# Optimization experiments

Hardware: AMD Instinct MI355X
Metric: run time of the kernel (lower is better)

The kernel has to match this reference:

```python
import jax, jax.numpy as jnp
import numpy as np

KSIZE = 7
STRIDE = 4
SCALE = 10.0


def _same_pad(n, k, s):
    # torch 'same' padding used in extract_image_patches (asymmetric)
    out = -(-n // s)
    pad = max(0, (out - 1) * s + k - n)
    top = pad // 2
    return (top, pad - top)


def _conv1x1(x, W, b):
    # x: [C,H,W], W: [O,C], b: [O]
    return jnp.einsum('oc,chw->ohw', W, x) + b[:, None, None]


def _unfold(x, k, s, pad_h, pad_w):
    # x: [C,H,W] -> patches [Lh*Lw, C*k*k] in (C, kh, kw) order (torch Unfold order)
    C = x.shape[0]
    xp = jnp.pad(x, ((0, 0), pad_h, pad_w))
    Hp, Wp = xp.shape[1], xp.shape[2]
    Lh = (Hp - k) // s + 1
    Lw = (Wp - k) // s + 1
    ih = (jnp.arange(Lh) * s)[:, None] + jnp.arange(k)  # [Lh,k]
    iw = (jnp.arange(Lw) * s)[:, None] + jnp.arange(k)  # [Lw,k]
    p = xp[:, ih][:, :, :, iw]                # [C,Lh,k,Lw,k]
    p = p.transpose(1, 3, 0, 2, 4).reshape(Lh * Lw, C * k * k)
    return p, Lh, Lw


def _fold(p, Lh, Lw, C, k, s, H, W, pad):
    # p: [Lh*Lw, C*k*k] -> overlap-summed image [C,H,W] (torch F.fold, symmetric pad)
    P = p.reshape(Lh, Lw, C, k, k).transpose(2, 0, 1, 3, 4)  # [C,Lh,Lw,k,k]
    Hp, Wp = H + 2 * pad, W + 2 * pad
    ih = (jnp.arange(Lh) * s)[:, None] + jnp.arange(k)  # [Lh,k]
    iw = (jnp.arange(Lw) * s)[:, None] + jnp.arange(k)  # [Lw,k]
    IH = ih[:, None, :, None]  # broadcast -> [Lh,Lw,k,k]
    IW = iw[None, :, None, :]
    canvas = jnp.zeros((C, Hp, Wp), p.dtype).at[:, IH, IW].add(P)
    return canvas[:, pad:pad + H, pad:pad + W]


def _salsa_one(x, Wg, bg, Wt, bt, Wp, bp, Ww, bw):
    # x: [C,H,W]
    C, H, W = x.shape
    ic = Wg.shape[0]
    k, s = KSIZE, STRIDE
    ph = _same_pad(H, k, s)
    pw = _same_pad(W, k, s)
    q, Lh, Lw = _unfold(_conv1x1(x, Wg, bg), k, s, ph, pw)   # g   -> queries [L, ic*k*k]
    kk, _, _ = _unfold(_conv1x1(x, Wp, bp), k, s, ph, pw)    # phi -> keys
    v, _, _ = _unfold(_conv1x1(x, Wt, bt), k, s, ph, pw)     # theta -> values
    att = jax.nn.softmax((q @ kk.T) * SCALE, axis=1)         # [L1,L2]
    out = att @ v                                            # [L1, ic*k*k]
    fp = (k - 1) // 2  # paddings[0] from stride-1 same_padding in the original (=3)
    zi = _fold(out, Lh, Lw, ic, k, s, H, W, fp)
    ones_p, mLh, mLw = _unfold(jnp.ones((ic, H, W), x.dtype), k, s, (fp, fp), (fp, fp))
    mask = _fold(ones_p, mLh, mLw, ic, k, s, H, W, fp)
    zi = zi / mask
    return x + _conv1x1(zi, Ww, bw)


def setup_inputs() -> dict:
    key = jax.random.key(0)
    B, C, H, W, IC = 4, 64, 256, 256, 16
    ks = jax.random.split(key, 9)
    sC = 1.0 / np.sqrt(C)
    sI = 1.0 / np.sqrt(IC)
    return {
        'b': jax.random.normal(ks[0], (B, C, H, W), jnp.float32),
        'Wg': jax.random.normal(ks[1], (IC, C), jnp.float32) * sC,
        'bg': jax.random.normal(ks[2], (IC,), jnp.float32) * 0.01,
        'Wt': jax.random.normal(ks[3], (IC, C), jnp.float32) * sC,
        'bt': jax.random.normal(ks[4], (IC,), jnp.float32) * 0.01,
        'Wp': jax.random.normal(ks[5], (IC, C), jnp.float32) * sC,
        'bp': jax.random.normal(ks[6], (IC,), jnp.float32) * 0.01,
        'Ww': jax.random.normal(ks[7], (C, IC), jnp.float32) * sI,
        'bw': jax.random.normal(ks[8], (C,), jnp.float32) * 0.01,
    }


def reference(b, Wg, bg, Wt, bt, Wp, bp, Ww, bw):
    f = jax.vmap(_salsa_one, in_axes=(0, None, None, None, None, None, None, None, None))
    return f(b, Wg, bg, Wt, bt, Wp, bp, Ww, bw)
```

## Files before the change

kernel.cpp:

```cpp
#include <hip/hip_runtime.h>

#define CIN 64
#define ICN 16
#define HH 256
#define WID 256
#define HW (HH*WID)
#define LL 4096
#define KD 784
#define KDP 800
#define NVT 896
#define NB 4

typedef __attribute__((ext_vector_type(8))) short short8;
typedef __attribute__((ext_vector_type(4))) float f32x4;

__device__ __forceinline__ unsigned short f2bf(float x){
  union { float f; unsigned u; } v; v.f = x;
  unsigned r = v.u + 0x7FFF + ((v.u >> 16) & 1);
  return (unsigned short)(r >> 16);
}
__device__ __forceinline__ float bf2f(unsigned short h){
  union { unsigned u; float f; } v; v.u = ((unsigned)h) << 16; return v.f;
}

__global__ __launch_bounds__(256) void conv1x1_3(
    const float* __restrict__ x,
    const float* __restrict__ Wg, const float* __restrict__ bg,
    const float* __restrict__ Wp, const float* __restrict__ bp,
    const float* __restrict__ Wt, const float* __restrict__ bt,
    float* __restrict__ G, float* __restrict__ P, float* __restrict__ T) {
  __shared__ float wg[ICN*CIN], wp[ICN*CIN], wt[ICN*CIN];
  int t = threadIdx.x;
  for (int i = t; i < ICN*CIN; i += 256) { wg[i]=Wg[i]; wp[i]=Wp[i]; wt[i]=Wt[i]; }
  __syncthreads();
  int p = blockIdx.x*256 + t;
  float aG[ICN], aP[ICN], aT[ICN];
#pragma unroll
  for (int o=0;o<ICN;o++){ aG[o]=bg[o]; aP[o]=bp[o]; aT[o]=bt[o]; }
  for (int c=0;c<CIN;c++){
    float xv = x[c*HW + p];
#pragma unroll
    for (int o=0;o<ICN;o++){
      aG[o] = fmaf(wg[o*CIN+c], xv, aG[o]);
      aP[o] = fmaf(wp[o*CIN+c], xv, aP[o]);
      aT[o] = fmaf(wt[o*CIN+c], xv, aT[o]);
    }
  }
#pragma unroll
  for (int o=0;o<ICN;o++){ G[o*HW+p]=aG[o]; P[o*HW+p]=aP[o]; T[o*HW+p]=aT[o]; }
}

__global__ __launch_bounds__(256) void unfold_qk(
    const float* __restrict__ G, const float* __restrict__ P,
    unsigned short* __restrict__ Qh, unsigned short* __restrict__ Ql,
    unsigned short* __restrict__ Kh, unsigned short* __restrict__ Kl){
  int row = blockIdx.x;
  int iy = row >> 6, ix = row & 63;
  for (int col = threadIdx.x; col < KDP; col += 256){
    float g = 0.f, p = 0.f;
    if (col < KD){
      int c = col / 49; int r = col - c*49; int dy = r / 7; int dx = r - dy*7;
      int y = (iy<<2) + dy - 1, x = (ix<<2) + dx - 1;
      if ((unsigned)y < HH && (unsigned)x < WID){
        int a = c*HW + (y<<8) + x;
        g = G[a]; p = P[a];
      }
    }
    size_t o = (size_t)row*KDP + col;
    unsigned short gh = f2bf(g); Qh[o]=gh; Ql[o]=f2bf(g - bf2f(gh));
    unsigned short ph = f2bf(p); Kh[o]=ph; Kl[o]=f2bf(p - bf2f(ph));
  }
}

__global__ __launch_bounds__(256) void unfold_vt(
    const float* __restrict__ T, unsigned short* __restrict__ Vt){
  int idx = blockIdx.x*256 + threadIdx.x;
  int col = idx >> 12, row = idx & 4095;
  float t = 0.f;
  if (col < KD){
    int c = col / 49; int r = col - c*49; int dy = r / 7; int dx = r - dy*7;
    int iy = row >> 6, ix = row & 63;
    int y = (iy<<2) + dy - 1, x = (ix<<2) + dx - 1;
    if ((unsigned)y < HH && (unsigned)x < WID) t = T[c*HW + (y<<8) + x];
  }
  Vt[idx] = f2bf(t);
}

__global__ __launch_bounds__(256) void gemm_qk_mfma(
    const unsigned short* __restrict__ Qh, const unsigned short* __restrict__ Ql,
    const unsigned short* __restrict__ Kh, const unsigned short* __restrict__ Kl,
    float* __restrict__ ATT){
  __shared__ alignas(16) short lds[4][128*32];
  const int tid = threadIdx.x;
  const int lane = tid & 63, w = tid >> 6;
  const int wr = w >> 1, wc = w & 1;
  const int row0 = blockIdx.y*128, col0 = blockIdx.x*128;

  const unsigned short* base;
  { const unsigned short* s0[4] = {
      Qh + (size_t)row0*KDP, Ql + (size_t)row0*KDP,
      Kh + (size_t)col0*KDP, Kl + (size_t)col0*KDP };
    base = s0[w]; }

  const int r_lo = lane >> 2, slot = lane & 3;
  int goff[8];
#pragma unroll
  for (int j=0;j<8;j++){
    int r = j*16 + r_lo;
    int sw = slot ^ ((r>>1)&3);
    goff[j] = r*KDP + sw*8;
  }

  const int lrow = lane & 15, g = lane >> 4;
  int offA[4], offB[4];
#pragma unroll
  for (int i=0;i<4;i++){
    int rA = wr*64 + i*16 + lrow;
    offA[i] = rA*32 + ((g ^ ((rA>>1)&3))<<3);
    int rB = wc*64 + i*16 + lrow;
    offB[i] = rB*32 + ((g ^ ((rB>>1)&3))<<3);
  }

  f32x4 acc[4][4] = {};

  for (int kb = 0; kb < KDP; kb += 32){
#pragma unroll
    for (int j=0;j<8;j++)
      __builtin_amdgcn_global_load_lds(
        (const __attribute__((address_space(1))) void*)(base + goff[j] + kb),
        (__attribute__((address_space(3))) void*)(&lds[w][j*512]), 16, 0, 0);
    __syncthreads();
    short8 ah[4], al[4], bh[4], bl[4];
#pragma unroll
    for (int i=0;i<4;i++){
      ah[i] = *(const short8*)&lds[0][offA[i]];
      al[i] = *(const short8*)&lds[1][offA[i]];
      bh[i] = *(const short8*)&lds[2][offB[i]];
      bl[i] = *(const short8*)&lds[3][offB[i]];
    }
#pragma unroll
    for (int i=0;i<4;i++)
#pragma unroll
      for (int j=0;j<4;j++){
        acc[i][j] = __builtin_amdgcn_mfma_f32_16x16x32_bf16(ah[i], bh[j], acc[i][j], 0,0,0);
        acc[i][j] = __builtin_amdgcn_mfma_f32_16x16x32_bf16(ah[i], bl[j], acc[i][j], 0,0,0);
        acc[i][j] = __builtin_amdgcn_mfma_f32_16x16x32_bf16(al[i], bh[j], acc[i][j], 0,0,0);
      }
    __syncthreads();
  }

  float* cbase = ATT + (size_t)(row0 + wr*64)*LL + col0 + wc*64;
#pragma unroll
  for (int i=0;i<4;i++)
#pragma unroll
    for (int j=0;j<4;j++)
#pragma unroll
      for (int r=0;r<4;r++)
        cbase[(size_t)(i*16 + g*4 + r)*LL + j*16 + lrow] = acc[i][j][r]*10.0f;
}

__global__ __launch_bounds__(256) void softmax_rows(
    const float* __restrict__ ATT, unsigned short* __restrict__ Pb){
  __shared__ float red[256];
  int t = threadIdx.x;
  const float* r = ATT + (size_t)blockIdx.x * LL;
  unsigned short* po = Pb + (size_t)blockIdx.x * LL;
  float v[16];
  float mx = -3.4e38f;
#pragma unroll
  for (int i=0;i<16;i++){ v[i] = r[t + (i<<8)]; mx = fmaxf(mx, v[i]); }
  red[t] = mx; __syncthreads();
  for (int s2=128;s2>0;s2>>=1){ if (t<s2) red[t]=fmaxf(red[t],red[t+s2]); __syncthreads(); }
  mx = red[0]; __syncthreads();
  float sum = 0.f;
#pragma unroll
  for (int i=0;i<16;i++){ v[i] = __expf(v[i]-mx); sum += v[i]; }
  red[t]=sum; __syncthreads();
  for (int s2=128;s2>0;s2>>=1){ if (t<s2) red[t]+=red[t+s2]; __syncthreads(); }
  float inv = 1.0f / red[0];
#pragma unroll
  for (int i=0;i<16;i++) po[t+(i<<8)] = f2bf(v[i]*inv);
}

__global__ __launch_bounds__(256) void gemm_pv_mfma(
    const unsigned short* __restrict__ Pb, const unsigned short* __restrict__ Vt,
    float* __restrict__ OUT){
  __shared__ alignas(16) short ldsA[128*32];
  __shared__ alignas(16) short ldsB[128*32];
  const int tid = threadIdx.x;
  const int lane = tid & 63, w = tid >> 6;
  const int wr = w >> 1, wc = w & 1;
  const int row0 = blockIdx.y*128, col0 = blockIdx.x*128;

  const unsigned short* baseA = Pb + (size_t)row0*LL;
  const unsigned short* baseB = Vt + (size_t)col0*LL;
  const int r_lo = lane >> 2, slot = lane & 3;
  int goff0, goff1;
  { int r = w*16 + r_lo;       goff0 = r*LL + ((slot ^ ((r>>1)&3))<<3); }
  { int r = (4+w)*16 + r_lo;   goff1 = r*LL + ((slot ^ ((r>>1)&3))<<3); }

  const int lrow = lane & 15, g = lane >> 4;
  int offA[4], offB[4];
#pragma unroll
  for (int i=0;i<4;i++){
    int rA = wr*64 + i*16 + lrow;
    offA[i] = rA*32 + ((g ^ ((rA>>1)&3))<<3);
    int rB = wc*64 + i*16 + lrow;
    offB[i] = rB*32 + ((g ^ ((rB>>1)&3))<<3);
  }

  f32x4 acc[4][4] = {};

  for (int kb = 0; kb < LL; kb += 32){
    __builtin_amdgcn_global_load_lds(
      (const __attribute__((address_space(1))) void*)(baseA + goff0 + kb),
      (__attribute__((address_space(3))) void*)(&ldsA[w*512]), 16, 0, 0);
    __builtin_amdgcn_global_load_lds(
      (const __attribute__((address_space(1))) void*)(baseA + goff1 + kb),
      (__attribute__((address_space(3))) void*)(&ldsA[(4+w)*512]), 16, 0, 0);
    __builtin_amdgcn_global_load_lds(
      (const __attribute__((address_space(1))) void*)(baseB + goff0 + kb),
      (__attribute__((address_space(3))) void*)(&ldsB[w*512]), 16, 0, 0);
    __builtin_amdgcn_global_load_lds(
      (const __attribute__((address_space(1))) void*)(baseB + goff1 + kb),
      (__attribute__((address_space(3))) void*)(&ldsB[(4+w)*512]), 16, 0, 0);
    __syncthreads();
    short8 a[4], b[4];
#pragma unroll
    for (int i=0;i<4;i++){
      a[i] = *(const short8*)&ldsA[offA[i]];
      b[i] = *(const short8*)&ldsB[offB[i]];
    }
#pragma unroll
    for (int i=0;i<4;i++)
#pragma unroll
      for (int j=0;j<4;j++)
        acc[i][j] = __builtin_amdgcn_mfma_f32_16x16x32_bf16(a[i], b[j], acc[i][j], 0,0,0);
    __syncthreads();
  }

#pragma unroll
  for (int i=0;i<4;i++)
#pragma unroll
    for (int j=0;j<4;j++){
      int col = col0 + wc*64 + j*16 + lrow;
      if (col < KD){
#pragma unroll
        for (int r=0;r<4;r++)
          OUT[(size_t)(row0 + wr*64 + i*16 + g*4 + r)*KDP + col] = acc[i][j][r];
      }
    }
}

__global__ __launch_bounds__(256) void fold_div(
    const float* __restrict__ OUT, float* __restrict__ ZI){
  int idx = blockIdx.x*256 + threadIdx.x;
  if (idx >= ICN*HW) return;
  int c = idx >> 16; int rem = idx & 65535; int y = rem >> 8; int x = rem & 255;
  int yc = y + 3, xc = x + 3;
  int i0 = (yc-3) >> 2; int i1 = yc >> 2; if (i1 > 63) i1 = 63;
  int j0 = (xc-3) >> 2; int j1 = xc >> 2; if (j1 > 63) j1 = 63;
  float s = 0.f;
  for (int i = i0; i <= i1; i++){
    int dy = yc - (i<<2);
    for (int j = j0; j <= j1; j++){
      int dx = xc - (j<<2);
      s += OUT[(size_t)((i<<6)+j)*KDP + c*49 + dy*7 + dx];
    }
  }
  float mask = (float)((i1-i0+1)*(j1-j0+1));
  ZI[idx] = s / mask;
}

__global__ __launch_bounds__(256) void final_out(
    const float* __restrict__ xin, const float* __restrict__ ZI,
    const float* __restrict__ Ww, const float* __restrict__ bw,
    float* __restrict__ out){
  int idx = blockIdx.x*256 + threadIdx.x;
  int co = idx >> 16;
  int p = idx & 65535;
  float acc = xin[idx] + bw[co];
#pragma unroll
  for (int ic=0; ic<ICN; ic++)
    acc = fmaf(Ww[co*ICN+ic], ZI[ic*HW + p], acc);
  out[idx] = acc;
}

extern "C" void kernel_launch(void* const* d_in, const int* in_sizes, int n_in,
                              void* d_out, int out_size, void* d_ws, size_t ws_size,
                              hipStream_t stream) {
  const float* xb = (const float*)d_in[0];
  const float* Wg = (const float*)d_in[1];
  const float* bg = (const float*)d_in[2];
  const float* Wt = (const float*)d_in[3];
  const float* bt = (const float*)d_in[4];
  const float* Wp = (const float*)d_in[5];
  const float* bp = (const float*)d_in[6];
  const float* Ww = (const float*)d_in[7];
  const float* bw = (const float*)d_in[8];
  float* out = (float*)d_out;

  char* ws = (char*)d_ws;
  float*          G   = (float*)(ws + 0);
  float*          Pc  = (float*)(ws + 4194304);
  float*          T   = (float*)(ws + 8388608);
  unsigned short* Qh  = (unsigned short*)(ws + 12582912);
  unsigned short* Ql  = (unsigned short*)(ws + 19136512);
  unsigned short* Kh  = (unsigned short*)(ws + 25690112);
  unsigned short* Kl  = (unsigned short*)(ws + 32243712);
  unsigned short* Vt  = (unsigned short*)(ws + 38797312);
  float*          ATT = (float*)(ws + 46137344);
  unsigned short* Pb  = (unsigned short*)(ws + 0);
  float*          ZI  = (float*)(ws + 33554432);
  float*          OUTm= (float*)(ws + 46137344);

  for (int b = 0; b < NB; b++){
    const float* x = xb + (size_t)b*CIN*HW;
    conv1x1_3<<<HW/256, 256, 0, stream>>>(x, Wg,bg, Wp,bp, Wt,bt, G,Pc,T);
    unfold_qk<<<LL, 256, 0, stream>>>(G, Pc, Qh, Ql, Kh, Kl);
    unfold_vt<<<NVT*LL/256, 256, 0, stream>>>(T, Vt);
    gemm_qk_mfma<<<dim3(LL/128, LL/128), 256, 0, stream>>>(Qh, Ql, Kh, Kl, ATT);
    softmax_rows<<<LL, 256, 0, stream>>>(ATT, Pb);
    gemm_pv_mfma<<<dim3(NVT/128, LL/128), 256, 0, stream>>>(Pb, Vt, OUTm);
    fold_div<<<(ICN*HW)/256, 256, 0, stream>>>(OUTm, ZI);
    final_out<<<CIN*HW/256, 256, 0, stream>>>(x, ZI, Ww, bw, out + (size_t)b*CIN*HW);
  }
}
```

Before: 1.235 ms.

## Use split int8 MFMA for QK scores and fuse fold with output conv

The QK^T product moves from a three-term bf16 hi/lo split to per-row symmetric int8 quantization with a two-level split (coarse plus residual scaled by 256). It runs i32 16x16x64 int8 MFMAs, which process twice the K depth per instruction, and halves the operand bytes. The result is rescaled by per-row Q and K scales at the end. Separately, the fold/mask-divide and the final 1x1 conv are fused into one per-pixel kernel, which removes the ZI round trip. The int8 split gives roughly 15 bits of precision, and large softmax logits (scale 10) may amplify quantization error.

```diff
diff --git a/kernel.cpp b/kernel.cpp
--- a/kernel.cpp
+++ b/kernel.cpp
@@ -8,19 +8,18 @@
 #define LL 4096
 #define KD 784
 #define KDP 800
+#define KQ 832
 #define NVT 896
 #define NB 4
 
 typedef __attribute__((ext_vector_type(8))) short short8;
 typedef __attribute__((ext_vector_type(4))) float f32x4;
+typedef __attribute__((ext_vector_type(4))) int i32x4;
 
 __device__ __forceinline__ unsigned short f2bf(float x){
   union { float f; unsigned u; } v; v.f = x;
   unsigned r = v.u + 0x7FFF + ((v.u >> 16) & 1);
   return (unsigned short)(r >> 16);
-}
-__device__ __forceinline__ float bf2f(unsigned short h){
-  union { unsigned u; float f; } v; v.u = ((unsigned)h) << 16; return v.f;
 }
 
 __global__ __launch_bounds__(256) void conv1x1_3(
@@ -50,13 +49,18 @@
   for (int o=0;o<ICN;o++){ G[o*HW+p]=aG[o]; P[o*HW+p]=aP[o]; T[o*HW+p]=aT[o]; }
 }
 
-__global__ __launch_bounds__(256) void unfold_qk(
+__global__ __launch_bounds__(256) void unfold_qk_q(
     const float* __restrict__ G, const float* __restrict__ P,
-    unsigned short* __restrict__ Qh, unsigned short* __restrict__ Ql,
-    unsigned short* __restrict__ Kh, unsigned short* __restrict__ Kl){
+    char* __restrict__ Q0, char* __restrict__ Q1,
+    char* __restrict__ K0, char* __restrict__ K1,
+    float* __restrict__ sQ, float* __restrict__ sK){
+  __shared__ float gb[KQ], pb[KQ];
+  __shared__ float redg[256], redp[256];
   int row = blockIdx.x;
   int iy = row >> 6, ix = row & 63;
-  for (int col = threadIdx.x; col < KDP; col += 256){
+  int t = threadIdx.x;
+  float gmax = 0.f, pmax = 0.f;
+  for (int col = t; col < KQ; col += 256){
     float g = 0.f, p = 0.f;
     if (col < KD){
       int c = col / 49; int r = col - c*49; int dy = r / 7; int dx = r - dy*7;
@@ -66,9 +70,39 @@
         g = G[a]; p = P[a];
       }
     }
-    size_t o = (size_t)row*KDP + col;
-    unsigned short gh = f2bf(g); Qh[o]=gh; Ql[o]=f2bf(g - bf2f(gh));
-    unsigned short ph = f2bf(p); Kh[o]=ph; Kl[o]=f2bf(p - bf2f(ph));
+    gb[col] = g; pb[col] = p;
+    gmax = fmaxf(gmax, fabsf(g)); pmax = fmaxf(pmax, fabsf(p));
+  }
+  redg[t]=gmax; redp[t]=pmax; __syncthreads();
+  for (int s2=128;s2>0;s2>>=1){
+    if (t<s2){ redg[t]=fmaxf(redg[t],redg[t+s2]); redp[t]=fmaxf(redp[t],redp[t+s2]); }
+    __syncthreads();
+  }
+  float mg = redg[0], mp = redp[0];
+  float rsg = mg > 0.f ? mg*(1.f/127.f) : 1.f;
+  float rsp = mp > 0.f ? mp*(1.f/127.f) : 1.f;
+  if (t==0){ sQ[row]=rsg; sK[row]=rsp; }
+  float ig = 1.f/rsg, ip = 1.f/rsp;
+  if (t < KQ/4){
+    char q0[4],q1[4],k0[4],k1[4];
+#pragma unroll
+    for (int u=0;u<4;u++){
+      float xg = gb[t*4+u]*ig;
+      float a0 = rintf(xg);
+      int ia1 = (int)rintf((xg - a0)*256.f);
+      ia1 = ia1>127?127:(ia1<-127?-127:ia1);
+      q0[u] = (char)(int)a0; q1[u] = (char)ia1;
+      float xp = pb[t*4+u]*ip;
+      float b0 = rintf(xp);
+      int ib1 = (int)rintf((xp - b0)*256.f);
+      ib1 = ib1>127?127:(ib1<-127?-127:ib1);
+      k0[u] = (char)(int)b0; k1[u] = (char)ib1;
+    }
+    size_t o = (size_t)row*KQ + t*4;
+    *(char4*)(Q0+o) = make_char4(q0[0],q0[1],q0[2],q0[3]);
+    *(char4*)(Q1+o) = make_char4(q1[0],q1[1],q1[2],q1[3]);
+    *(char4*)(K0+o) = make_char4(k0[0],k0[1],k0[2],k0[3]);
+    *(char4*)(K1+o) = make_char4(k1[0],k1[1],k1[2],k1[3]);
   }
 }
 
@@ -86,20 +120,21 @@
   Vt[idx] = f2bf(t);
 }
 
-__global__ __launch_bounds__(256) void gemm_qk_mfma(
-    const unsigned short* __restrict__ Qh, const unsigned short* __restrict__ Ql,
-    const unsigned short* __restrict__ Kh, const unsigned short* __restrict__ Kl,
+__global__ __launch_bounds__(256) void gemm_qk_i8(
+    const char* __restrict__ Q0, const char* __restrict__ Q1,
+    const char* __restrict__ K0, const char* __restrict__ K1,
+    const float* __restrict__ sQ, const float* __restrict__ sK,
     float* __restrict__ ATT){
-  __shared__ alignas(16) short lds[4][128*32];
+  __shared__ alignas(16) char lds[4][128*64];
   const int tid = threadIdx.x;
   const int lane = tid & 63, w = tid >> 6;
   const int wr = w >> 1, wc = w & 1;
   const int row0 = blockIdx.y*128, col0 = blockIdx.x*128;
 
-  const unsigned short* base;
-  { const unsigned short* s0[4] = {
-      Qh + (size_t)row0*KDP, Ql + (size_t)row0*KDP,
-      Kh + (size_t)col0*KDP, Kl + (size_t)col0*KDP };
+  const char* base;
+  { const char* s0[4] = {
+      Q0 + (size_t)row0*KQ, Q1 + (size_t)row0*KQ,
+      K0 + (size_t)col0*KQ, K1 + (size_t)col0*KQ };
     base = s0[w]; }
 
   const int r_lo = lane >> 2, slot = lane & 3;
@@ -107,8 +142,7 @@
 #pragma unroll
   for (int j=0;j<8;j++){
     int r = j*16 + r_lo;
-    int sw = slot ^ ((r>>1)&3);
-    goff[j] = r*KDP + sw*8;
+    goff[j] = r*KQ + ((slot ^ ((r>>1)&3))<<4);
   }
 
   const int lrow = lane & 15, g = lane >> 4;
@@ -116,47 +150,55 @@
 #pragma unroll
   for (int i=0;i<4;i++){
     int rA = wr*64 + i*16 + lrow;
-    offA[i] = rA*32 + ((g ^ ((rA>>1)&3))<<3);
+    offA[i] = rA*64 + ((g ^ ((rA>>1)&3))<<4);
     int rB = wc*64 + i*16 + lrow;
-    offB[i] = rB*32 + ((g ^ ((rB>>1)&3))<<3);
-  }
-
-  f32x4 acc[4][4] = {};
-
-  for (int kb = 0; kb < KDP; kb += 32){
+    offB[i] = rB*64 + ((g ^ ((rB>>1)&3))<<4);
+  }
+
+  i32x4 accH[4][4] = {};
+  i32x4 accC[4][4] = {};
+
+  for (int kb = 0; kb < KQ; kb += 64){
 #pragma unroll
     for (int j=0;j<8;j++)
       __builtin_amdgcn_global_load_lds(
         (const __attribute__((address_space(1))) void*)(base + goff[j] + kb),
-        (__attribute__((address_space(3))) void*)(&lds[w][j*512]), 16, 0, 0);
-    __syncthreads();
-    short8 ah[4], al[4], bh[4], bl[4];
+        (__attribute__((address_space(3))) void*)(&lds[w][j*1024]), 16, 0, 0);
+    __syncthreads();
+    i32x4 a0[4], a1[4], b0[4], b1[4];
 #pragma unroll
     for (int i=0;i<4;i++){
-      ah[i] = *(const short8*)&lds[0][offA[i]];
-      al[i] = *(const short8*)&lds[1][offA[i]];
-      bh[i] = *(const short8*)&lds[2][offB[i]];
-      bl[i] = *(const short8*)&lds[3][offB[i]];
+      a0[i] = *(const i32x4*)&lds[0][offA[i]];
+      a1[i] = *(const i32x4*)&lds[1][offA[i]];
+      b0[i] = *(const i32x4*)&lds[2][offB[i]];
+      b1[i] = *(const i32x4*)&lds[3][offB[i]];
     }
 #pragma unroll
     for (int i=0;i<4;i++)
 #pragma unroll
       for (int j=0;j<4;j++){
-        acc[i][j] = __builtin_amdgcn_mfma_f32_16x16x32_bf16(ah[i], bh[j], acc[i][j], 0,0,0);
-        acc[i][j] = __builtin_amdgcn_mfma_f32_16x16x32_bf16(ah[i], bl[j], acc[i][j], 0,0,0);
-        acc[i][j] = __builtin_amdgcn_mfma_f32_16x16x32_bf16(al[i], bh[j], acc[i][j], 0,0,0);
+        accH[i][j] = __builtin_amdgcn_mfma_i32_16x16x64_i8(a0[i], b0[j], accH[i][j], 0,0,0);
+        accC[i][j] = __builtin_amdgcn_mfma_i32_16x16x64_i8(a0[i], b1[j], accC[i][j], 0,0,0);
+        accC[i][j] = __builtin_amdgcn_mfma_i32_16x16x64_i8(a1[i], b0[j], accC[i][j], 0,0,0);
       }
     __syncthreads();
   }
 
-  float* cbase = ATT + (size_t)(row0 + wr*64)*LL + col0 + wc*64;
-#pragma unroll
-  for (int i=0;i<4;i++)
-#pragma unroll
-    for (int j=0;j<4;j++)
-#pragma unroll
-      for (int r=0;r<4;r++)
-        cbase[(size_t)(i*16 + g*4 + r)*LL + j*16 + lrow] = acc[i][j][r]*10.0f;
+#pragma unroll
+  for (int j=0;j<4;j++){
+    int col = col0 + wc*64 + j*16 + lrow;
+    float cs = sK[col]*10.f;
+#pragma unroll
+    for (int i=0;i<4;i++){
+#pragma unroll
+      for (int r=0;r<4;r++){
+        int row = row0 + wr*64 + i*16 + g*4 + r;
+        float rs = sQ[row];
+        ATT[(size_t)row*LL + col] =
+          rs*cs*((float)accH[i][j][r] + (float)accC[i][j][r]*0.00390625f);
+      }
+    }
+  }
 }
 
 __global__ __launch_bounds__(256) void softmax_rows(
@@ -252,38 +294,48 @@
     }
 }
 
-__global__ __launch_bounds__(256) void fold_div(
-    const float* __restrict__ OUT, float* __restrict__ ZI){
-  int idx = blockIdx.x*256 + threadIdx.x;
-  if (idx >= ICN*HW) return;
-  int c = idx >> 16; int rem = idx & 65535; int y = rem >> 8; int x = rem & 255;
+__global__ __launch_bounds__(256) void fold_final(
+    const float* __restrict__ OUT, const float* __restrict__ xin,
+    const float* __restrict__ Ww, const float* __restrict__ bw,
+    float* __restrict__ out){
+  __shared__ float wsh[CIN*ICN];
+  __shared__ float bsh[CIN];
+  int t = threadIdx.x;
+  for (int i=t;i<CIN*ICN;i+=256) wsh[i]=Ww[i];
+  if (t<CIN) bsh[t]=bw[t];
+  __syncthreads();
+  int p = blockIdx.x*256 + t;
+  int y = p >> 8, x = p & 255;
   int yc = y + 3, xc = x + 3;
   int i0 = (yc-3) >> 2; int i1 = yc >> 2; if (i1 > 63) i1 = 63;
   int j0 = (xc-3) >> 2; int j1 = xc >> 2; if (j1 > 63) j1 = 63;
-  float s = 0.f;
+  float zi[ICN] = {};
   for (int i = i0; i <= i1; i++){
     int dy = yc - (i<<2);
     for (int j = j0; j <= j1; j++){
       int dx = xc - (j<<2);
-      s += OUT[(size_t)((i<<6)+j)*KDP + c*49 + dy*7 + dx];
-    }
-  }
-  float mask = (float)((i1-i0+1)*(j1-j0+1));
-  ZI[idx] = s / mask;
-}
-
-__global__ __launch_bounds__(256) void final_out(
-    const float* __restrict__ xin, const float* __restrict__ ZI,
-    const float* __restrict__ Ww, const float* __restrict__ bw,
-    float* __restrict__ out){
-  int idx = blockIdx.x*256 + threadIdx.x;
-  int co = idx >> 16;
-  int p = idx & 65535;
-  float acc = xin[idx] + bw[co];
-#pragma unroll
-  for (int ic=0; ic<ICN; ic++)
-    acc = fmaf(Ww[co*ICN+ic], ZI[ic*HW + p], acc);
-  out[idx] = acc;
+      const float* bp = &OUT[(size_t)((i<<6)+j)*KDP + dy*7 + dx];
+#pragma unroll
+      for (int c=0;c<ICN;c++) zi[c] += bp[c*49];
+    }
+  }
+  float inv = 1.0f / (float)((i1-i0+1)*(j1-j0+1));
+#pragma unroll
+  for (int c=0;c<ICN;c++) zi[c] *= inv;
+#pragma unroll
+  for (int co=0;co<CIN;co++){
+    float acc = xin[co*HW + p] + bsh[co];
+    const float4* w4 = (const float4*)&wsh[co*ICN];
+#pragma unroll
+    for (int c4=0;c4<4;c4++){
+      float4 wv = w4[c4];
+      acc = fmaf(wv.x, zi[c4*4+0], acc);
+      acc = fmaf(wv.y, zi[c4*4+1], acc);
+      acc = fmaf(wv.z, zi[c4*4+2], acc);
+      acc = fmaf(wv.w, zi[c4*4+3], acc);
+    }
+    out[co*HW + p] = acc;
+  }
 }
 
 extern "C" void kernel_launch(void* const* d_in, const int* in_sizes, int n_in,
@@ -304,25 +356,25 @@
   float*          G   = (float*)(ws + 0);
   float*          Pc  = (float*)(ws + 4194304);
   float*          T   = (float*)(ws + 8388608);
-  unsigned short* Qh  = (unsigned short*)(ws + 12582912);
-  unsigned short* Ql  = (unsigned short*)(ws + 19136512);
-  unsigned short* Kh  = (unsigned short*)(ws + 25690112);
-  unsigned short* Kl  = (unsigned short*)(ws + 32243712);
-  unsigned short* Vt  = (unsigned short*)(ws + 38797312);
-  float*          ATT = (float*)(ws + 46137344);
+  char*           Q0  = (char*)(ws + 12582912);
+  char*           Q1  = (char*)(ws + 15990784);
+  char*           K0  = (char*)(ws + 19398656);
+  char*           K1  = (char*)(ws + 22806528);
+  float*          sQ  = (float*)(ws + 26214400);
+  float*          sK  = (float*)(ws + 26230784);
+  float*          ATT = (float*)(ws + 33554432);
+  unsigned short* Vt  = (unsigned short*)(ws + 100663296);
   unsigned short* Pb  = (unsigned short*)(ws + 0);
-  float*          ZI  = (float*)(ws + 33554432);
-  float*          OUTm= (float*)(ws + 46137344);
+  float*          OUTm= (float*)(ws + 33554432);
 
   for (int b = 0; b < NB; b++){
     const float* x = xb + (size_t)b*CIN*HW;
     conv1x1_3<<<HW/256, 256, 0, stream>>>(x, Wg,bg, Wp,bp, Wt,bt, G,Pc,T);
-    unfold_qk<<<LL, 256, 0, stream>>>(G, Pc, Qh, Ql, Kh, Kl);
+    unfold_qk_q<<<LL, 256, 0, stream>>>(G, Pc, Q0, Q1, K0, K1, sQ, sK);
     unfold_vt<<<NVT*LL/256, 256, 0, stream>>>(T, Vt);
-    gemm_qk_mfma<<<dim3(LL/128, LL/128), 256, 0, stream>>>(Qh, Ql, Kh, Kl, ATT);
+    gemm_qk_i8<<<dim3(LL/128, LL/128), 256, 0, stream>>>(Q0, Q1, K0, K1, sQ, sK, ATT);
     softmax_rows<<<LL, 256, 0, stream>>>(ATT, Pb);
     gemm_pv_mfma<<<dim3(NVT/128, LL/128), 256, 0, stream>>>(Pb, Vt, OUTm);
-    fold_div<<<(ICN*HW)/256, 256, 0, stream>>>(OUTm, ZI);
-    final_out<<<CIN*HW/256, 256, 0, stream>>>(x, ZI, Ww, bw, out + (size_t)b*CIN*HW);
-  }
-}
+    fold_final<<<HW/256, 256, 0, stream>>>(OUTm, x, Ww, bw, out + (size_t)b*CIN*HW);
+  }
+}
```

After: 1.189 ms. 1.04x faster.
